# Performance work log

Measured on AMD Instinct MI355X. Metric: run time of the kernel, lower is better.

## Reference

```python
import jax, jax.numpy as jnp
import numpy as np

B, T = 256, 2048
D = 64           # rnn_embd_dims (== input_dims)
LB = 2           # len(band_names)
DB = D // LB     # band_embedding_dims = 32
L = 2            # rnn_layers
G = 3 * DB       # GRU gate width


def setup_inputs() -> dict:
    key = jax.random.key(0)
    ks = jax.random.split(key, 10)
    s = 0.1
    return {
        "band_ids": jax.random.randint(ks[0], (B, T), 0, LB),
        "dtime": jax.random.uniform(ks[1], (B, T, 1), dtype=jnp.float32),
        "z_last": jax.random.normal(ks[2], (B, D), dtype=jnp.float32),
        # per-band params stacked on a leading band axis
        "proj_W": jax.random.normal(ks[3], (LB, D + 1, DB)) * s,
        "proj_b": jnp.zeros((LB, DB)),
        "Wih": jax.random.normal(ks[4], (LB, L, G, DB)) * s,
        "Whh": jax.random.normal(ks[5], (LB, L, G, DB)) * s,
        "bih": jnp.zeros((LB, L, G)),
        "bhh": jnp.zeros((LB, L, G)),
        "mW1": jax.random.normal(ks[6], (LB, DB, DB)) * s,
        "mb1": jnp.zeros((LB, DB)),
        "mW2": jax.random.normal(ks[7], (LB, DB, 1)) * s,
        "mb2": jnp.zeros((LB, 1)),
    }


def _gru_layer(x, mask, Wih, Whh, bih, bhh):
    # x: [B,T,DB], mask: [B,T] bool (True = valid step; invalid steps keep h)
    gx = jnp.einsum('btd,gd->btg', x, Wih) + bih  # precompute input gates [B,T,3*DB]

    def step(h, inp):
        gx_t, m_t = inp                 # [B,G], [B]
        gh = h @ Whh.T + bhh            # [B,G]
        r = jax.nn.sigmoid(gx_t[:, :DB] + gh[:, :DB])
        z = jax.nn.sigmoid(gx_t[:, DB:2 * DB] + gh[:, DB:2 * DB])
        n = jnp.tanh(gx_t[:, 2 * DB:] + r * gh[:, 2 * DB:])
        hn = (1.0 - z) * n + z * h
        h = jnp.where(m_t[:, None], hn, h)
        return h, h

    h0 = jnp.zeros((x.shape[0], DB), x.dtype)
    _, ys = jax.lax.scan(step, h0, (gx.transpose(1, 0, 2), mask.T))
    return ys.transpose(1, 0, 2)  # [B,T,DB]


def _forward(band_ids, dtime, z_last, proj_W, proj_b, Wih, Whh, bih, bhh, mW1, mb1, mW2, mb2):
    Bn, Tn = band_ids.shape
    outs = []
    for kb in range(LB):
        mask = band_ids == kb  # [B,T]
        # serial_to_parallel: stable-compact valid steps to the front of each row
        order = jnp.argsort(jnp.logical_not(mask), axis=1, stable=True)
        p_mask = jnp.take_along_axis(mask, order, axis=1)
        p_dtime = jnp.take_along_axis(dtime, order[:, :, None], axis=1)
        # dz = z_last tiled over t; gather along t is identity for a t-constant tensor
        p_dz = jnp.broadcast_to(z_last[:, None, :], (Bn, Tn, z_last.shape[-1]))
        x = jnp.concatenate([p_dz, p_dtime], axis=-1) @ proj_W[kb] + proj_b[kb]
        for l in range(L):
            x = _gru_layer(x, p_mask, Wih[kb, l], Whh[kb, l], bih[kb, l], bhh[kb, l])
        # dz_projection MLP: hidden relu layer + linear head -> [B,T,1]
        y = jax.nn.relu(x @ mW1[kb] + mb1[kb]) @ mW2[kb] + mb2[kb]
        outs.append(y)
    return tuple(outs)


def reference(band_ids, dtime, z_last, proj_W, proj_b, Wih, Whh, bih, bhh, mW1, mb1, mW2, mb2):
    return _forward(band_ids, dtime, z_last, proj_W, proj_b, Wih, Whh, bih, bhh, mW1, mb1, mW2, mb2)
```

## Files before the change

### kernel.cpp

```cpp
#include <hip/hip_runtime.h>


typedef float v2f __attribute__((ext_vector_type(2)));

constexpr int Bn  = 256;
constexpr int Tn  = 2048;
constexpr int Dn  = 64;
constexpr int DBn = 32;
constexpr int Ln  = 2;
constexpr int Gn  = 96;
constexpr int Kc  = 16;

#if __has_builtin(__builtin_amdgcn_exp2f)
__device__ __forceinline__ float exp2_fast(float x) { return __builtin_amdgcn_exp2f(x); }
#else
__device__ __forceinline__ float exp2_fast(float x) { return exp2f(x); }
#endif
#if __has_builtin(__builtin_amdgcn_rcpf)
__device__ __forceinline__ float rcp_fast(float x) { return __builtin_amdgcn_rcpf(x); }
#else
__device__ __forceinline__ float rcp_fast(float x) { return 1.0f / x; }
#endif

__device__ __forceinline__ float sigmoid_f(float x) {
  return rcp_fast(1.0f + exp2_fast(-1.4426950408889634f * x));
}
__device__ __forceinline__ float tanh_f(float x) {
  return 1.0f - 2.0f * rcp_fast(1.0f + exp2_fast(2.8853900817779268f * x));
}

template <int CTRL>
__device__ __forceinline__ float dpp_add(float x) {
  int y = __builtin_amdgcn_update_dpp(0, __builtin_bit_cast(int, x), CTRL, 0xf, 0xf, true);
  return x + __builtin_bit_cast(float, y);
}
__device__ __forceinline__ float dppx8_add(float x) { return dpp_add<0x128>(x); }
__device__ __forceinline__ float dpp_row_sum16(float x) {
  x = dpp_add<0x128>(x);
  x = dpp_add<0x124>(x);
  x = dpp_add<0x122>(x);
  x = dpp_add<0x121>(x);
  return x;
}

__device__ __forceinline__ float dot8(const v2f* __restrict__ w, const v2f* __restrict__ h) {
  v2f a = {0.0f, 0.0f};
  #pragma unroll
  for (int q = 0; q < 8; ++q) a = __builtin_elementwise_fma(w[q], h[q], a);
  return a.x + a.y;
}
__device__ __forceinline__ float dot8b(const v2f* __restrict__ w, const v2f* __restrict__ h) {
  v2f a = {0.0f, 0.0f}, b = {0.0f, 0.0f};
  #pragma unroll
  for (int q = 0; q < 4; ++q) {
    a = __builtin_elementwise_fma(w[q], h[q], a);
    b = __builtin_elementwise_fma(w[q + 4], h[q + 4], b);
  }
  a = a + b;
  return a.x + a.y;
}

__device__ __forceinline__ void ld16(const float* p, v2f* d) {
  #pragma unroll
  for (int q = 0; q < 4; ++q) {
    float4 a = ((const float4*)p)[q];
    d[2*q] = (v2f){a.x, a.y}; d[2*q+1] = (v2f){a.z, a.w};
  }
}

__global__ __launch_bounds__(256, 1)
void rnn_decoder(const int* __restrict__ band_ids, const float* __restrict__ dtime,
                 const float* __restrict__ z_last, const float* __restrict__ projW,
                 const float* __restrict__ projB, const float* __restrict__ Wih,
                 const float* __restrict__ Whh, const float* __restrict__ bih,
                 const float* __restrict__ bhh, const float* __restrict__ mW1,
                 const float* __restrict__ mb1, const float* __restrict__ mW2,
                 const float* __restrict__ mb2, float* __restrict__ out) {
  const int b    = blockIdx.x >> 1;
  const int kb   = blockIdx.x & 1;
  const int tid  = threadIdx.x;
  const int wv   = tid >> 6;
  const int w    = wv ^ ((blockIdx.x >> 8) & 1);
  const int L    = tid & 63;
  const int e    = (L & 7) | ((L >> 4) << 3);
  const int koff = ((L >> 3) & 1) * 16;

  __shared__ __align__(16) float yd[Tn];
  __shared__ __align__(16) float gxr_[2][Kc][DBn][4];
  __shared__ __align__(16) float h1r_[2][Kc][DBn];
  __shared__ __align__(16) float h2r_[2][Kc][DBn];
  __shared__ __align__(16) float vr_[2][Kc][4];
  __shared__ __align__(16) float xb[DBn], xs[DBn];
  __shared__ int nsh;

  const float mb2v = mb2[kb];

  if (w == 0) {
    {
      const int*   brow = band_ids + b * Tn;
      const float* drow = dtime    + b * Tn;
      int cnt = 0;
      int4 bcache[8];
      #pragma unroll
      for (int it = 0; it < 8; ++it) {
        int4 v = ((const int4*)(brow + L * 32))[it];
        bcache[it] = v;
        cnt += (v.x == kb) + (v.y == kb) + (v.z == kb) + (v.w == kb);
      }
      int incl = cnt;
      #pragma unroll
      for (int dlt = 1; dlt < 64; dlt <<= 1) {
        int v = __shfl_up(incl, dlt, 64);
        if (L >= dlt) incl += v;
      }
      int off = incl - cnt;
      const int n0 = __shfl(incl, 63, 64);
      #pragma unroll
      for (int it = 0; it < 8; ++it) {
        int4   v  = bcache[it];
        float4 dd = ((const float4*)(drow + L * 32))[it];
        if (v.x == kb) yd[off++] = dd.x;
        if (v.y == kb) yd[off++] = dd.y;
        if (v.z == kb) yd[off++] = dd.z;
        if (v.w == kb) yd[off++] = dd.w;
      }
      if (L == 0) nsh = n0;
    }
    {
      const float* pw = projW + (kb * (Dn + 1)) * DBn + e;
      const float* zl = z_last + b * Dn;
      float acc = 0.0f;
      #pragma unroll 8
      for (int k = 0; k < Dn; ++k) acc = fmaf(zl[k], pw[k * DBn], acc);
      xb[e] = acc + projB[kb * DBn + e];
      xs[e] = pw[Dn * DBn];
    }
    __builtin_amdgcn_wave_barrier();
    const float* wih1  = Wih + ((kb * Ln + 0) * Gn) * DBn;
    const float* bih1p = bih + (kb * Ln + 0) * Gn;
    const float* bhh1p = bhh + (kb * Ln + 0) * Gn;
    float gb_r = 0, gb_z = 0, gb_n = 0, gs_r = 0, gs_z = 0, gs_n = 0;
    #pragma unroll 4
    for (int j = 0; j < DBn; ++j) {
      float xbv = xb[j], xsv = xs[j];
      float wr = wih1[(     e) * DBn + j];
      float wz = wih1[(32 + e) * DBn + j];
      float wn = wih1[(64 + e) * DBn + j];
      gb_r = fmaf(wr, xbv, gb_r);  gs_r = fmaf(wr, xsv, gs_r);
      gb_z = fmaf(wz, xbv, gb_z);  gs_z = fmaf(wz, xsv, gs_z);
      gb_n = fmaf(wn, xbv, gb_n);  gs_n = fmaf(wn, xsv, gs_n);
    }
    gb_r += bih1p[e]      + bhh1p[e];
    gb_z += bih1p[32 + e] + bhh1p[32 + e];
    gb_n += bih1p[64 + e];
    const float bhh1n = bhh1p[64 + e];
    v2f w1r[8], w1z[8], w1n[8];
    const float* whh1 = Whh + ((kb * Ln + 0) * Gn) * DBn;
    ld16(whh1 + (     e) * DBn + koff, w1r);
    ld16(whh1 + (32 + e) * DBn + koff, w1z);
    ld16(whh1 + (64 + e) * DBn + koff, w1n);
    __syncthreads();

#if __has_builtin(__builtin_amdgcn_s_setprio)
    __builtin_amdgcn_s_setprio(1);
#endif
    const int n = nsh;
    const int C = (n + Kc - 1) >> 4;
    v2f h1a[8];
    #pragma unroll
    for (int q = 0; q < 8; ++q) h1a[q] = (v2f){0.0f, 0.0f};
    float h1self = 0.0f;
    for (int c = 0; c < C + 4; ++c) {
      if (c < C) {
        float* ring = &h1r_[c & 1][0][0];
        const int t0 = c * Kc;
        for (int k = 0; k < Kc; ++k) {
          float d  = yd[t0 + k];
          float ar = dot8b(w1r, h1a);
          float az = dot8b(w1z, h1a);
          float an = dot8b(w1n, h1a);
          ar = dppx8_add(ar);
          az = dppx8_add(az);
          an = dppx8_add(an);
          float r1 = sigmoid_f(fmaf(d, gs_r, gb_r) + ar);
          float z1 = sigmoid_f(fmaf(d, gs_z, gb_z) + az);
          float n1 = tanh_f(fmaf(d, gs_n, gb_n) + r1 * (an + bhh1n));
          h1self = fmaf(z1, h1self - n1, n1);
          ring[k * DBn + e] = h1self;
          __builtin_amdgcn_wave_barrier();
          ld16(&ring[k * DBn + koff], h1a);
        }
      }
      __syncthreads();
    }
  } else if (w == 1) {
    const float* wih2 = Wih + ((kb * Ln + 1) * Gn) * DBn;
    v2f wa[8], wbv[8], wcv[8];
    ld16(wih2 + (     e) * DBn + koff, wa);
    ld16(wih2 + (32 + e) * DBn + koff, wbv);
    ld16(wih2 + (64 + e) * DBn + koff, wcv);
    __syncthreads();

    const int n = nsh;
    const int C = (n + Kc - 1) >> 4;
    for (int c = 0; c < C + 4; ++c) {
      if (c >= 1 && c <= C) {
        const int cp = c - 1;
        const float* hsrc = &h1r_[cp & 1][0][0];
        for (int k = 0; k < Kc; ++k) {
          v2f hb[8];
          ld16(&hsrc[k * DBn + koff], hb);
          float g0 = dot8(wa,  hb);
          float g1 = dot8(wbv, hb);
          float g2 = dot8(wcv, hb);
          g0 = dppx8_add(g0);
          g1 = dppx8_add(g1);
          g2 = dppx8_add(g2);
          float4 gv; gv.x = g0; gv.y = g1; gv.z = g2; gv.w = 0.0f;
          *(float4*)&gxr_[cp & 1][k][e][0] = gv;
        }
      }
      if (c >= 4) {
        const int cd = c - 4;
        if (cd < C && L < Kc) {
          float4 p = *(const float4*)&vr_[cd & 1][L][0];
          yd[cd * Kc + L] = ((p.x + p.y) + (p.z + p.w)) + mb2v;
        }
      }
      __syncthreads();
    }
  } else if (w == 2) {
    const float* whh2  = Whh + ((kb * Ln + 1) * Gn) * DBn;
    const float* bih2p = bih + (kb * Ln + 1) * Gn;
    const float* bhh2p = bhh + (kb * Ln + 1) * Gn;
    v2f r2w[8], z2w[8], n2w[8];
    ld16(whh2 + (     e) * DBn + koff, r2w);
    ld16(whh2 + (32 + e) * DBn + koff, z2w);
    ld16(whh2 + (64 + e) * DBn + koff, n2w);
    const float c2r   = bih2p[e]      + bhh2p[e];
    const float c2z   = bih2p[32 + e] + bhh2p[32 + e];
    const float bih2n = bih2p[64 + e];
    const float bhh2n = bhh2p[64 + e];
    __syncthreads();

#if __has_builtin(__builtin_amdgcn_s_setprio)
    __builtin_amdgcn_s_setprio(1);
#endif
    const int n = nsh;
    const int C = (n + Kc - 1) >> 4;
    v2f h2a[8];
    #pragma unroll
    for (int q = 0; q < 8; ++q) h2a[q] = (v2f){0.0f, 0.0f};
    float h2self = 0.0f;
    for (int c = 0; c < C + 4; ++c) {
      if (c >= 2 && c <= C + 1) {
        const int cc = c - 2;
        float* ring = &h2r_[cc & 1][0][0];
        for (int k = 0; k < Kc; ++k) {
          float4 g = *(const float4*)&gxr_[cc & 1][k][e][0];
          float cr = dot8b(r2w, h2a);
          float cz = dot8b(z2w, h2a);
          float cn = dot8b(n2w, h2a);
          cr = dppx8_add(cr);
          cz = dppx8_add(cz);
          cn = dppx8_add(cn);
          float r2v = sigmoid_f(g.x + cr + c2r);
          float z2v = sigmoid_f(g.y + cz + c2z);
          float n2v = tanh_f(g.z + bih2n + r2v * (cn + bhh2n));
          h2self = fmaf(z2v, h2self - n2v, n2v);
          ring[k * DBn + e] = h2self;
          __builtin_amdgcn_wave_barrier();
          ld16(&ring[k * DBn + koff], h2a);
        }
      }
      __syncthreads();
    }
  } else {
    v2f m1c[8];
    #pragma unroll
    for (int q = 0; q < 8; ++q)
      m1c[q] = (v2f){ mW1[(kb * DBn + koff + 2*q)     * DBn + e],
                      mW1[(kb * DBn + koff + 2*q + 1) * DBn + e] };
    const float mb1e = mb1[kb * DBn + e];
    const float mW2h = 0.5f * mW2[kb * DBn + e];
    {
      float p = fmaxf(mb1e, 0.0f) * mW2h;
      p = dpp_row_sum16(p);
      if ((L & 15) == 15) vr_[0][0][L >> 4] = p;
    }
    __syncthreads();

    const int n = nsh;
    const int C = (n + Kc - 1) >> 4;
    for (int c = 0; c < C + 4; ++c) {
      if (c >= 3 && c <= C + 2) {
        const int cm = c - 3;
        const float* hsrc = &h2r_[cm & 1][0][0];
        for (int k = 0; k < Kc; ++k) {
          v2f hb[8];
          ld16(&hsrc[k * DBn + koff], hb);
          float mh = dot8(m1c, hb);
          mh = dppx8_add(mh);
          float v = fmaxf(mh + mb1e, 0.0f) * mW2h;
          v = dpp_row_sum16(v);
          if ((L & 15) == 15) vr_[cm & 1][k][L >> 4] = v;
        }
      }
      __syncthreads();
    }
  }

  const int n = nsh;
  float ylast;
  if (n > 0) {
    ylast = yd[n - 1];
  } else {
    float4 p = *(const float4*)&vr_[0][0][0];
    ylast = ((p.x + p.y) + (p.z + p.w)) + mb2v;
  }
  for (int t = n + tid; t < Tn; t += 256) yd[t] = ylast;
  __syncthreads();

  float* orow = out + (kb * Bn + b) * Tn;
  for (int q = tid; q < Tn / 4; q += 256)
    ((float4*)orow)[q] = ((const float4*)yd)[q];
}

extern "C" void kernel_launch(void* const* d_in, const int* in_sizes, int n_in,
                              void* d_out, int out_size, void* d_ws, size_t ws_size,
                              hipStream_t stream) {
  const int*   band_ids = (const int*)  d_in[0];
  const float* dtime    = (const float*)d_in[1];
  const float* z_last   = (const float*)d_in[2];
  const float* projW    = (const float*)d_in[3];
  const float* projB    = (const float*)d_in[4];
  const float* Wih      = (const float*)d_in[5];
  const float* Whh      = (const float*)d_in[6];
  const float* bihp     = (const float*)d_in[7];
  const float* bhhp     = (const float*)d_in[8];
  const float* mW1      = (const float*)d_in[9];
  const float* mb1      = (const float*)d_in[10];
  const float* mW2      = (const float*)d_in[11];
  const float* mb2      = (const float*)d_in[12];
  float* out = (float*)d_out;
  rnn_decoder<<<dim3(Bn * 2), dim3(256), 0, stream>>>(
      band_ids, dtime, z_last, projW, projB, Wih, Whh, bihp, bhhp,
      mW1, mb1, mW2, mb2, out);
}
```

Measured before the change: 372.3 us.

## Process both bands per block with 8 waves and fuse layer-2 input gates

```diff
diff --git a/kernel.cpp b/kernel.cpp
--- a/kernel.cpp
+++ b/kernel.cpp
@@ -9,7 +9,7 @@
 constexpr int DBn = 32;
 constexpr int Ln  = 2;
 constexpr int Gn  = 96;
-constexpr int Kc  = 16;
+constexpr int Kc  = 32;
 
 #if __has_builtin(__builtin_amdgcn_exp2f)
 __device__ __forceinline__ float exp2_fast(float x) { return __builtin_amdgcn_exp2f(x); }
@@ -68,7 +68,7 @@
   }
 }
 
-__global__ __launch_bounds__(256, 1)
+__global__ __launch_bounds__(512, 2)
 void rnn_decoder(const int* __restrict__ band_ids, const float* __restrict__ dtime,
                  const float* __restrict__ z_last, const float* __restrict__ projW,
                  const float* __restrict__ projB, const float* __restrict__ Wih,
@@ -76,64 +76,71 @@
                  const float* __restrict__ bhh, const float* __restrict__ mW1,
                  const float* __restrict__ mb1, const float* __restrict__ mW2,
                  const float* __restrict__ mb2, float* __restrict__ out) {
-  const int b    = blockIdx.x >> 1;
-  const int kb   = blockIdx.x & 1;
+  const int b    = blockIdx.x;
   const int tid  = threadIdx.x;
   const int wv   = tid >> 6;
-  const int w    = wv ^ ((blockIdx.x >> 8) & 1);
   const int L    = tid & 63;
   const int e    = (L & 7) | ((L >> 4) << 3);
   const int koff = ((L >> 3) & 1) * 16;
 
-  __shared__ __align__(16) float yd[Tn];
-  __shared__ __align__(16) float gxr_[2][Kc][DBn][4];
-  __shared__ __align__(16) float h1r_[2][Kc][DBn];
-  __shared__ __align__(16) float h2r_[2][Kc][DBn];
-  __shared__ __align__(16) float vr_[2][Kc][4];
-  __shared__ __align__(16) float xb[DBn], xs[DBn];
-  __shared__ int nsh;
-
-  const float mb2v = mb2[kb];
-
-  if (w == 0) {
-    {
-      const int*   brow = band_ids + b * Tn;
-      const float* drow = dtime    + b * Tn;
-      int cnt = 0;
-      int4 bcache[8];
-      #pragma unroll
-      for (int it = 0; it < 8; ++it) {
-        int4 v = ((const int4*)(brow + L * 32))[it];
-        bcache[it] = v;
-        cnt += (v.x == kb) + (v.y == kb) + (v.z == kb) + (v.w == kb);
-      }
-      int incl = cnt;
-      #pragma unroll
-      for (int dlt = 1; dlt < 64; dlt <<= 1) {
-        int v = __shfl_up(incl, dlt, 64);
-        if (L >= dlt) incl += v;
-      }
-      int off = incl - cnt;
-      const int n0 = __shfl(incl, 63, 64);
-      #pragma unroll
-      for (int it = 0; it < 8; ++it) {
-        int4   v  = bcache[it];
-        float4 dd = ((const float4*)(drow + L * 32))[it];
-        if (v.x == kb) yd[off++] = dd.x;
-        if (v.y == kb) yd[off++] = dd.y;
-        if (v.z == kb) yd[off++] = dd.z;
-        if (v.w == kb) yd[off++] = dd.w;
-      }
-      if (L == 0) nsh = n0;
-    }
+  int role, bn;
+  if (wv < 2)      { role = 0; bn = wv; }
+  else if (wv < 4) { role = 1; bn = wv - 2; }
+  else if (wv < 6) { role = 2; bn = 5 - wv; }
+  else             { role = 3; bn = wv - 6; }
+  const int kb = bn;
+
+  __shared__ __align__(16) float yd[2][Tn];
+  __shared__ __align__(16) float h1r[2][2][Kc][DBn];
+  __shared__ __align__(16) float h2r[2][2][Kc][DBn];
+  __shared__ __align__(16) float vr[2][2][Kc][4];
+  __shared__ __align__(16) float xb[2][DBn], xs[2][DBn];
+  __shared__ int nsh[2];
+  __shared__ float ldspad[8192];
+  if (tid == 0) ((volatile float*)ldspad)[0] = 0.0f;
+
+  if (role == 3) {
+    const int*   brow = band_ids + b * Tn;
+    const float* drow = dtime    + b * Tn;
+    int cnt = 0;
+    int4 bcache[8];
+    #pragma unroll
+    for (int it = 0; it < 8; ++it) {
+      int4 v = ((const int4*)(brow + L * 32))[it];
+      bcache[it] = v;
+      cnt += (v.x == kb) + (v.y == kb) + (v.z == kb) + (v.w == kb);
+    }
+    int incl = cnt;
+    #pragma unroll
+    for (int dlt = 1; dlt < 64; dlt <<= 1) {
+      int v = __shfl_up(incl, dlt, 64);
+      if (L >= dlt) incl += v;
+    }
+    int off = incl - cnt;
+    const int nb0 = __shfl(incl, 63, 64);
+    #pragma unroll
+    for (int it = 0; it < 8; ++it) {
+      int4   v  = bcache[it];
+      float4 dd = ((const float4*)(drow + L * 32))[it];
+      if (v.x == kb) yd[bn][off++] = dd.x;
+      if (v.y == kb) yd[bn][off++] = dd.y;
+      if (v.z == kb) yd[bn][off++] = dd.z;
+      if (v.w == kb) yd[bn][off++] = dd.w;
+    }
+    if (L == 0) nsh[bn] = nb0;
+    __syncthreads();
+    const int CM = (((nsh[0] + Kc - 1) >> 5) > ((nsh[1] + Kc - 1) >> 5))
+                     ? ((nsh[0] + Kc - 1) >> 5) : ((nsh[1] + Kc - 1) >> 5);
+    for (int c = 0; c < CM + 3; ++c) __syncthreads();
+  } else if (role == 0) {
     {
       const float* pw = projW + (kb * (Dn + 1)) * DBn + e;
       const float* zl = z_last + b * Dn;
       float acc = 0.0f;
       #pragma unroll 8
       for (int k = 0; k < Dn; ++k) acc = fmaf(zl[k], pw[k * DBn], acc);
-      xb[e] = acc + projB[kb * DBn + e];
-      xs[e] = pw[Dn * DBn];
+      xb[bn][e] = acc + projB[kb * DBn + e];
+      xs[bn][e] = pw[Dn * DBn];
     }
     __builtin_amdgcn_wave_barrier();
     const float* wih1  = Wih + ((kb * Ln + 0) * Gn) * DBn;
@@ -142,7 +149,7 @@
     float gb_r = 0, gb_z = 0, gb_n = 0, gs_r = 0, gs_z = 0, gs_n = 0;
     #pragma unroll 4
     for (int j = 0; j < DBn; ++j) {
-      float xbv = xb[j], xsv = xs[j];
+      float xbv = xb[bn][j], xsv = xs[bn][j];
       float wr = wih1[(     e) * DBn + j];
       float wz = wih1[(32 + e) * DBn + j];
       float wn = wih1[(64 + e) * DBn + j];
@@ -164,18 +171,20 @@
 #if __has_builtin(__builtin_amdgcn_s_setprio)
     __builtin_amdgcn_s_setprio(1);
 #endif
-    const int n = nsh;
-    const int C = (n + Kc - 1) >> 4;
+    const int C0 = (nsh[0] + Kc - 1) >> 5, C1 = (nsh[1] + Kc - 1) >> 5;
+    const int CM = C0 > C1 ? C0 : C1;
+    const int Cb = bn ? C1 : C0;
+    const float* ydb = &yd[bn][0];
     v2f h1a[8];
     #pragma unroll
     for (int q = 0; q < 8; ++q) h1a[q] = (v2f){0.0f, 0.0f};
     float h1self = 0.0f;
-    for (int c = 0; c < C + 4; ++c) {
-      if (c < C) {
-        float* ring = &h1r_[c & 1][0][0];
+    for (int c = 0; c < CM + 3; ++c) {
+      if (c < Cb) {
+        float* ring = &h1r[bn][c & 1][0][0];
         const int t0 = c * Kc;
         for (int k = 0; k < Kc; ++k) {
-          float d  = yd[t0 + k];
+          float d  = ydb[t0 + k];
           float ar = dot8b(w1r, h1a);
           float az = dot8b(w1z, h1a);
           float an = dot8b(w1n, h1a);
@@ -193,43 +202,12 @@
       }
       __syncthreads();
     }
-  } else if (w == 1) {
+  } else if (role == 1) {
     const float* wih2 = Wih + ((kb * Ln + 1) * Gn) * DBn;
     v2f wa[8], wbv[8], wcv[8];
     ld16(wih2 + (     e) * DBn + koff, wa);
     ld16(wih2 + (32 + e) * DBn + koff, wbv);
     ld16(wih2 + (64 + e) * DBn + koff, wcv);
-    __syncthreads();
-
-    const int n = nsh;
-    const int C = (n + Kc - 1) >> 4;
-    for (int c = 0; c < C + 4; ++c) {
-      if (c >= 1 && c <= C) {
-        const int cp = c - 1;
-        const float* hsrc = &h1r_[cp & 1][0][0];
-        for (int k = 0; k < Kc; ++k) {
-          v2f hb[8];
-          ld16(&hsrc[k * DBn + koff], hb);
-          float g0 = dot8(wa,  hb);
-          float g1 = dot8(wbv, hb);
-          float g2 = dot8(wcv, hb);
-          g0 = dppx8_add(g0);
-          g1 = dppx8_add(g1);
-          g2 = dppx8_add(g2);
-          float4 gv; gv.x = g0; gv.y = g1; gv.z = g2; gv.w = 0.0f;
-          *(float4*)&gxr_[cp & 1][k][e][0] = gv;
-        }
-      }
-      if (c >= 4) {
-        const int cd = c - 4;
-        if (cd < C && L < Kc) {
-          float4 p = *(const float4*)&vr_[cd & 1][L][0];
-          yd[cd * Kc + L] = ((p.x + p.y) + (p.z + p.w)) + mb2v;
-        }
-      }
-      __syncthreads();
-    }
-  } else if (w == 2) {
     const float* whh2  = Whh + ((kb * Ln + 1) * Gn) * DBn;
     const float* bih2p = bih + (kb * Ln + 1) * Gn;
     const float* bhh2p = bhh + (kb * Ln + 1) * Gn;
@@ -246,27 +224,33 @@
 #if __has_builtin(__builtin_amdgcn_s_setprio)
     __builtin_amdgcn_s_setprio(1);
 #endif
-    const int n = nsh;
-    const int C = (n + Kc - 1) >> 4;
+    const int C0 = (nsh[0] + Kc - 1) >> 5, C1 = (nsh[1] + Kc - 1) >> 5;
+    const int CM = C0 > C1 ? C0 : C1;
+    const int Cb = bn ? C1 : C0;
     v2f h2a[8];
     #pragma unroll
     for (int q = 0; q < 8; ++q) h2a[q] = (v2f){0.0f, 0.0f};
     float h2self = 0.0f;
-    for (int c = 0; c < C + 4; ++c) {
-      if (c >= 2 && c <= C + 1) {
-        const int cc = c - 2;
-        float* ring = &h2r_[cc & 1][0][0];
+    for (int c = 0; c < CM + 3; ++c) {
+      if (c >= 1 && c - 1 < Cb) {
+        const int cc = c - 1;
+        const float* hsrc = &h1r[bn][cc & 1][0][0];
+        float* ring = &h2r[bn][cc & 1][0][0];
         for (int k = 0; k < Kc; ++k) {
-          float4 g = *(const float4*)&gxr_[cc & 1][k][e][0];
+          v2f hb[8];
+          ld16(&hsrc[k * DBn + koff], hb);
+          float g0 = dppx8_add(dot8(wa,  hb));
+          float g1 = dppx8_add(dot8(wbv, hb));
+          float g2 = dppx8_add(dot8(wcv, hb));
           float cr = dot8b(r2w, h2a);
           float cz = dot8b(z2w, h2a);
           float cn = dot8b(n2w, h2a);
           cr = dppx8_add(cr);
           cz = dppx8_add(cz);
           cn = dppx8_add(cn);
-          float r2v = sigmoid_f(g.x + cr + c2r);
-          float z2v = sigmoid_f(g.y + cz + c2z);
-          float n2v = tanh_f(g.z + bih2n + r2v * (cn + bhh2n));
+          float r2v = sigmoid_f(g0 + cr + c2r);
+          float z2v = sigmoid_f(g1 + cz + c2z);
+          float n2v = tanh_f(g2 + bih2n + r2v * (cn + bhh2n));
           h2self = fmaf(z2v, h2self - n2v, n2v);
           ring[k * DBn + e] = h2self;
           __builtin_amdgcn_wave_barrier();
@@ -283,47 +267,60 @@
                       mW1[(kb * DBn + koff + 2*q + 1) * DBn + e] };
     const float mb1e = mb1[kb * DBn + e];
     const float mW2h = 0.5f * mW2[kb * DBn + e];
+    const float mb2v = mb2[kb];
     {
       float p = fmaxf(mb1e, 0.0f) * mW2h;
       p = dpp_row_sum16(p);
-      if ((L & 15) == 15) vr_[0][0][L >> 4] = p;
+      if ((L & 15) == 15) vr[bn][0][0][L >> 4] = p;
     }
     __syncthreads();
 
-    const int n = nsh;
-    const int C = (n + Kc - 1) >> 4;
-    for (int c = 0; c < C + 4; ++c) {
-      if (c >= 3 && c <= C + 2) {
-        const int cm = c - 3;
-        const float* hsrc = &h2r_[cm & 1][0][0];
+    const int C0 = (nsh[0] + Kc - 1) >> 5, C1 = (nsh[1] + Kc - 1) >> 5;
+    const int CM = C0 > C1 ? C0 : C1;
+    const int Cb = bn ? C1 : C0;
+    float* ydb = &yd[bn][0];
+    for (int c = 0; c < CM + 3; ++c) {
+      if (c >= 2 && c - 2 < Cb) {
+        const int cm = c - 2;
+        const float* hsrc = &h2r[bn][cm & 1][0][0];
         for (int k = 0; k < Kc; ++k) {
           v2f hb[8];
           ld16(&hsrc[k * DBn + koff], hb);
-          float mh = dot8(m1c, hb);
-          mh = dppx8_add(mh);
+          float mh = dppx8_add(dot8(m1c, hb));
           float v = fmaxf(mh + mb1e, 0.0f) * mW2h;
           v = dpp_row_sum16(v);
-          if ((L & 15) == 15) vr_[cm & 1][k][L >> 4] = v;
+          if ((L & 15) == 15) vr[bn][cm & 1][k][L >> 4] = v;
+        }
+      }
+      if (c >= 3) {
+        const int cd = c - 3;
+        if (cd < Cb && L < Kc) {
+          float4 p = *(const float4*)&vr[bn][cd & 1][L][0];
+          ydb[cd * Kc + L] = ((p.x + p.y) + (p.z + p.w)) + mb2v;
         }
       }
       __syncthreads();
     }
   }
 
-  const int n = nsh;
+  const int band = tid >> 8;
+  const int ct   = tid & 255;
+  const int nf   = nsh[band];
+  const float mb2e = mb2[band];
   float ylast;
-  if (n > 0) {
-    ylast = yd[n - 1];
+  if (nf > 0) {
+    ylast = yd[band][nf - 1];
   } else {
-    float4 p = *(const float4*)&vr_[0][0][0];
-    ylast = ((p.x + p.y) + (p.z + p.w)) + mb2v;
+    float4 p = *(const float4*)&vr[band][0][0][0];
+    ylast = ((p.x + p.y) + (p.z + p.w)) + mb2e;
   }
-  for (int t = n + tid; t < Tn; t += 256) yd[t] = ylast;
+  for (int t = nf + ct; t < Tn; t += 256) yd[band][t] = ylast;
   __syncthreads();
 
-  float* orow = out + (kb * Bn + b) * Tn;
-  for (int q = tid; q < Tn / 4; q += 256)
-    ((float4*)orow)[q] = ((const float4*)yd)[q];
+  float* orow = out + (band * Bn + b) * Tn;
+  #pragma unroll 2
+  for (int q = ct; q < Tn / 4; q += 256)
+    ((float4*)orow)[q] = ((const float4*)&yd[band][0])[q];
 }
 
 extern "C" void kernel_launch(void* const* d_in, const int* in_sizes, int n_in,
@@ -343,7 +340,7 @@
   const float* mW2      = (const float*)d_in[11];
   const float* mb2      = (const float*)d_in[12];
   float* out = (float*)d_out;
-  rnn_decoder<<<dim3(Bn * 2), dim3(256), 0, stream>>>(
+  rnn_decoder<<<dim3(Bn), dim3(512), 0, stream>>>(
       band_ids, dtime, z_last, projW, projB, Wih, Whh, bihp, bhhp,
       mW1, mb1, mW2, mb2, out);
 }
```

New measurement: 368.8 us. Within noise of the previous version (-0.9%).
